# Kernel optimization log

Measured on AMD Instinct MI355X. Metric: run time of the kernel, lower is better.

The kernel has to match this reference:

```python
import jax, jax.numpy as jnp
import numpy as np
from jax import lax

DIM = 128
HEADS = 4
B, H, W = 8, 128, 128


def conv1x1(x, w, b):
    # x: [B,C,H,W], w: [O,I,1,1]
    y = lax.conv_general_dilated(x, w, (1, 1), 'VALID',
                                 dimension_numbers=('NCHW', 'OIHW', 'NCHW'))
    return y + b[None, :, None, None]


def dwconv3x3(x, w, b):
    # depthwise: w: [C,1,3,3], groups=C
    C = x.shape[1]
    y = lax.conv_general_dilated(x, w, (1, 1), ((1, 1), (1, 1)),
                                 dimension_numbers=('NCHW', 'OIHW', 'NCHW'),
                                 feature_group_count=C)
    return y + b[None, :, None, None]


def setup_inputs() -> dict:
    key = jax.random.key(0)
    ks = jax.random.split(key, 7)
    s = 0.02
    return {
        'x': jax.random.normal(ks[0], (B, DIM, H, W), jnp.float32),
        'qkv_w': jax.random.normal(ks[1], (3 * DIM, DIM, 1, 1), jnp.float32) * s,
        'qkv_b': jnp.zeros((3 * DIM,), jnp.float32),
        'dw_w': jax.random.normal(ks[2], (3 * DIM, 1, 3, 3), jnp.float32) * s,
        'dw_b': jnp.zeros((3 * DIM,), jnp.float32),
        'proj_w': jax.random.normal(ks[3], (DIM, DIM, 1, 1), jnp.float32) * s,
        'proj_b': jnp.zeros((DIM,), jnp.float32),
        'temperature': jnp.ones((HEADS, 1, 1, 1), jnp.float32),
    }


def reference(x, qkv_w, qkv_b, dw_w, dw_b, proj_w, proj_b, temperature):
    b, C, h, w = x.shape
    heads = temperature.shape[0]
    c = C // heads

    qkv = dwconv3x3(conv1x1(x, qkv_w, qkv_b), dw_w, dw_b)
    q, k, v = jnp.split(qkv, 3, axis=1)

    # b (head c) h w -> b head c h w
    q = q.reshape(b, heads, c, h, w)
    k = k.reshape(b, heads, c, h, w)
    v = v.reshape(b, heads, c, h, w)

    # L2-normalize along H (axis=-2), matching torch F.normalize eps=1e-12
    eps = 1e-12
    q = q / jnp.maximum(jnp.linalg.norm(q, axis=-2, keepdims=True), eps)
    k = k / jnp.maximum(jnp.linalg.norm(k, axis=-2, keepdims=True), eps)

    # attn[b,n,c,j,k] = sum_i q[b,n,c,i,j] * k_[b,n,c,i,k]  -> [b,head,c,W,W]
    attn = jnp.einsum('bncij,bncik->bncjk', q, k) * temperature
    attn = jax.nn.softmax(attn, axis=-2)

    # out[b,n,c,i,k] = sum_j v[b,n,c,i,j] * attn[b,n,c,j,k]
    out = jnp.einsum('bncij,bncjk->bncik', v, attn)
    out = out.reshape(b, C, h, w)
    return conv1x1(out, proj_w, proj_b)
```

## Files before the change

### kernel.cpp

```cpp
#include <hip/hip_runtime.h>

typedef unsigned short u16;
typedef unsigned int   u32;

typedef short bf16x8 __attribute__((ext_vector_type(8)));
typedef float f32x4  __attribute__((ext_vector_type(4)));

__device__ __forceinline__ float bf2f(u16 u) { return __uint_as_float(((u32)u) << 16); }
__device__ __forceinline__ u16 f2bf(float f) {
    u32 u = __float_as_uint(f);
    return (u16)((u + 0x7fffu + ((u >> 16) & 1u)) >> 16);
}

#define MFMA16(a, b, c) __builtin_amdgcn_mfma_f32_16x16x32_bf16(a, b, c, 0, 0, 0)

__global__ __launch_bounds__(256, 4) void k_xpose(const float* __restrict__ x,
                                                  u16* __restrict__ xT) {
    __shared__ u16 Xs[128 * 128];
    const int ptile = blockIdx.x, b = blockIdx.y;
    const int t = threadIdx.x;
    const float* xb = x + (((size_t)b) << 21) + ptile * 128;
#pragma unroll
    for (int i = 0; i < 16; ++i) {
        int idx = i * 256 + t;
        int ci = idx >> 5, pq = idx & 31;
        float4 v = *(const float4*)(xb + (((size_t)ci) << 14) + pq * 4);
        u32 lo = (u32)f2bf(v.x) | ((u32)f2bf(v.y) << 16);
        u32 hi = (u32)f2bf(v.z) | ((u32)f2bf(v.w) << 16);
        uint2 pk; pk.x = lo; pk.y = hi;
        int cq = ci >> 3;
        *(uint2*)(&Xs[ci * 128 + ((pq ^ cq) << 2)]) = pk;
    }
    __syncthreads();
    u16* ob = xT + (((size_t)b) << 21) + ((size_t)(ptile * 128)) * 128;
#pragma unroll
    for (int j = 0; j < 8; ++j) {
        int p = j * 16 + (t >> 4), cq = t & 15;
        u16 tmp[8];
#pragma unroll
        for (int c = 0; c < 8; ++c) {
            int ci = cq * 8 + c;
            tmp[c] = Xs[ci * 128 + (((p >> 2) ^ cq) << 2) + (p & 3)];
        }
        *(uint4*)(&ob[(size_t)p * 128 + cq * 8]) = *(const uint4*)tmp;
    }
}

__global__ __launch_bounds__(512, 6) void k_qkv(const u16* __restrict__ xT,
                                                const float* __restrict__ w,
                                                const float* __restrict__ bias,
                                                u16* __restrict__ out1) {
    extern __shared__ char smem[];
    u16* Bt = (u16*)smem;
    u16* Cs = Bt + 2048 * 8;
    const int h = blockIdx.x, cg = blockIdx.y, b = blockIdx.z;
    const int t = threadIdx.x;

    const u16* xb = xT + (((size_t)b) << 21) + ((size_t)(h * 128)) * 128;
#pragma unroll
    for (int i = 0; i < 4; ++i) {
        int slot = i * 512 + t;
        int p = slot >> 4, g = slot & 15;
        int gg = g ^ (p & 15);
        uint4 v = *(const uint4*)(&xb[p * 128 + gg * 8]);
        *(uint4*)(&Bt[slot * 8]) = v;
    }

    const int wave = t >> 6, lane = t & 63, m16 = lane & 15, quad = lane >> 4;
    bf16x8 afr[4];
    {
        const float* wp0 = w + (size_t)(cg * 128 + wave * 16 + m16) * 128 + quad * 8;
#pragma unroll
        for (int kk = 0; kk < 4; ++kk) {
            float4 w0 = *(const float4*)(wp0 + kk * 32);
            float4 w1 = *(const float4*)(wp0 + kk * 32 + 4);
            bf16x8 a;
            a[0] = (short)f2bf(w0.x); a[1] = (short)f2bf(w0.y);
            a[2] = (short)f2bf(w0.z); a[3] = (short)f2bf(w0.w);
            a[4] = (short)f2bf(w1.x); a[5] = (short)f2bf(w1.y);
            a[6] = (short)f2bf(w1.z); a[7] = (short)f2bf(w1.w);
            afr[kk] = a;
        }
    }
    __syncthreads();

    f32x4 acc[8] = {};
#pragma unroll
    for (int kk = 0; kk < 4; ++kk) {
        const int g = kk * 4 + quad;
#pragma unroll
        for (int nt = 0; nt < 8; ++nt) {
            int p = nt * 16 + m16;
            bf16x8 bf = *(const bf16x8*)(&Bt[p * 128 + ((g ^ (p & 15)) << 3)]);
            acc[nt] = MFMA16(afr[kk], bf, acc[nt]);
        }
    }

    float bv[4];
#pragma unroll
    for (int r = 0; r < 4; ++r) bv[r] = bias[cg * 128 + wave * 16 + quad * 4 + r];

    u16* ob = out1 + (((size_t)(b * 384 + cg * 128)) << 14) + (h << 7);

    if (wave < 4) {
#pragma unroll
        for (int nt = 0; nt < 8; ++nt) {
            int p = nt * 16 + m16;
#pragma unroll
            for (int r = 0; r < 4; ++r)
                Cs[(wave * 16 + quad * 4 + r) * 136 + p] = f2bf(acc[nt][r] + bv[r]);
        }
    }
    __syncthreads();
#pragma unroll
    for (int it = 0; it < 2; ++it) {
        int idx = it * 512 + t;
        int co = idx >> 4, cp = idx & 15;
        *(uint4*)(&ob[((size_t)co << 14) + cp * 8]) = *(const uint4*)(&Cs[co * 136 + cp * 8]);
    }
    __syncthreads();

    if (wave >= 4) {
#pragma unroll
        for (int nt = 0; nt < 8; ++nt) {
            int p = nt * 16 + m16;
#pragma unroll
            for (int r = 0; r < 4; ++r)
                Cs[((wave - 4) * 16 + quad * 4 + r) * 136 + p] = f2bf(acc[nt][r] + bv[r]);
        }
    }
    __syncthreads();
    u16* ob2 = ob + ((size_t)64 << 14);
#pragma unroll
    for (int it = 0; it < 2; ++it) {
        int idx = it * 512 + t;
        int co = idx >> 4, cp = idx & 15;
        *(uint4*)(&ob2[((size_t)co << 14) + cp * 8]) = *(const uint4*)(&Cs[co * 136 + cp * 8]);
    }
}

__global__ __launch_bounds__(512, 4) void k_attn(const u16* __restrict__ qkv,
                                                 const float* __restrict__ dww,
                                                 const float* __restrict__ dwb,
                                                 const float* __restrict__ temp,
                                                 u16* __restrict__ outp) {
    extern __shared__ char smem[];
    u16* Qt = (u16*)smem;
    u16* Kt = Qt + 16384;
    u16* Vr = (u16*)smem;
    u16* Sg2 = Qt + 32768;
    float* ps = (float*)(smem + 75904);
    float* rq = (float*)(smem + 77952);
    float* rk = (float*)(smem + 78464);
    u16* Pt = Qt;
    u16* Osh = Kt;

    const int ch = blockIdx.x, b = blockIdx.y;
    const int head = ch >> 5;
    const int t = threadIdx.x;
    const size_t qoff = ((size_t)(b * 384 + ch)) << 14;
    const size_t koff = qoff + ((size_t)128 << 14);
    const size_t voff = qoff + ((size_t)256 << 14);

    const int wave = t >> 6, lane = t & 63, m16 = lane & 15, quad = lane >> 4;

#pragma unroll
    for (int i = 0; i < 4; ++i) {
        int idx = i * 512 + t;
        int r = idx >> 4, c16 = idx & 15;
        *(uint4*)(&Vr[r * 144 + 8 + c16 * 8]) =
            *(const uint4*)(&qkv[voff + ((size_t)r << 7) + c16 * 8]);
    }
    if (t < 256) {
        int r = t >> 1, side = t & 1;
        uint4 z = {0, 0, 0, 0};
        *(uint4*)(&Vr[r * 144 + side * 136]) = z;
    } else if (t < 328) {
        int i = t - 256;
        int row = i >> 1, side = i & 1;
        uint4 z = {0, 0, 0, 0};
        *(uint4*)(&Sg2[row * 144 + side * 136]) = z;
    }
    __syncthreads();

    bf16x8 vfr[4];
    {
        float wv9[9];
        const float* wp = dww + (size_t)(256 + ch) * 9;
#pragma unroll
        for (int i = 0; i < 9; ++i) wv9[i] = wp[i];
        const float bvv = dwb[256 + ch];
        const int r = wave * 16 + m16;
#pragma unroll
        for (int kk = 0; kk < 4; ++kk) {
            const int c0 = quad * 8 + kk * 32;
            float acc[8];
#pragma unroll
            for (int c = 0; c < 8; ++c) acc[c] = bvv;
#pragma unroll
            for (int dy = 0; dy < 3; ++dy) {
                int rr = r + dy - 1;
                if ((unsigned)rr < 128u) {
                    const u16* row = &Vr[rr * 144 + 8 + c0];
                    float v0 = bf2f(row[-1]);
                    uint4 m = *(const uint4*)row;
                    float v1 = bf2f((u16)(m.x & 0xffff)), v2 = bf2f((u16)(m.x >> 16));
                    float v3 = bf2f((u16)(m.y & 0xffff)), v4 = bf2f((u16)(m.y >> 16));
                    float v5 = bf2f((u16)(m.z & 0xffff)), v6 = bf2f((u16)(m.z >> 16));
                    float v7 = bf2f((u16)(m.w & 0xffff)), v8 = bf2f((u16)(m.w >> 16));
                    float v9 = bf2f(row[8]);
                    const float w0 = wv9[dy * 3], w1 = wv9[dy * 3 + 1], w2 = wv9[dy * 3 + 2];
                    acc[0] += w0 * v0 + w1 * v1 + w2 * v2;
                    acc[1] += w0 * v1 + w1 * v2 + w2 * v3;
                    acc[2] += w0 * v2 + w1 * v3 + w2 * v4;
                    acc[3] += w0 * v3 + w1 * v4 + w2 * v5;
                    acc[4] += w0 * v4 + w1 * v5 + w2 * v6;
                    acc[5] += w0 * v5 + w1 * v6 + w2 * v7;
                    acc[6] += w0 * v6 + w1 * v7 + w2 * v8;
                    acc[7] += w0 * v7 + w1 * v8 + w2 * v9;
                }
            }
            bf16x8 a;
#pragma unroll
            for (int c = 0; c < 8; ++c) a[c] = (short)f2bf(acc[c]);
            vfr[kk] = a;
        }
    }
    __syncthreads();

    const int gmat = t >> 8, gig = (t >> 7) & 1, gj = t & 127;
    u16* gdstbase = (gmat ? Kt : Qt) + gj * 128;
    float wg9[9];
    {
        const float* wp = dww + (size_t)((gmat ? 128 : 0) + ch) * 9;
#pragma unroll
        for (int i = 0; i < 9; ++i) wg9[i] = wp[i];
    }
    const float gb = dwb[(gmat ? 128 : 0) + ch];
    float ssq = 0.f;

#pragma unroll 1
    for (int p = 0; p < 8; ++p) {
#pragma unroll
        for (int s0 = 0; s0 < 2; ++s0) {
            int s = s0 * 512 + t;
            if (s < 576) {
                int m = (s >= 288) ? 1 : 0;
                int within = s - m * 288;
                int lr = within >> 4, c16 = within & 15;
                int hh = p * 16 - 1 + lr;
                uint4 v = {0, 0, 0, 0};
                if ((unsigned)hh < 128u)
                    v = *(const uint4*)(&qkv[(m ? koff : qoff) + ((size_t)hh << 7) + c16 * 8]);
                *(uint4*)(&Sg2[(m * 18 + lr) * 144 + 8 + c16 * 8]) = v;
            }
        }
        __syncthreads();

        const u16* colp = &Sg2[(gmat * 18 + gig * 8) * 144 + 8 + gj];
        float acc[8];
#pragma unroll
        for (int c = 0; c < 8; ++c) acc[c] = gb;
#pragma unroll
        for (int lr = 0; lr < 10; ++lr) {
            const u16* rp = colp + lr * 144;
            float L = bf2f(rp[-1]);
            float C = bf2f(rp[0]);
            float R = bf2f(rp[1]);
            if (lr < 8) {
                float s0v = wg9[0] * L + wg9[1] * C + wg9[2] * R;
                acc[lr] += s0v;
            }
            if (lr >= 1 && lr <= 8) {
                float s1v = wg9[3] * L + wg9[4] * C + wg9[5] * R;
                acc[lr - 1] += s1v;
            }
            if (lr >= 2) {
                float s2v = wg9[6] * L + wg9[7] * C + wg9[8] * R;
                acc[lr - 2] += s2v;
            }
        }
        u16 tmp[8];
#pragma unroll
        for (int c = 0; c < 8; ++c) {
            u16 uv = f2bf(acc[c]);
            tmp[c] = uv;
            float f = bf2f(uv);
            ssq += f * f;
        }
        int g = p * 2 + gig;
        *(uint4*)(gdstbase + ((g ^ (gj & 15)) << 3)) = *(const uint4*)tmp;
        __syncthreads();
    }

    ps[(gmat * 2 + gig) * 128 + gj] = ssq;
    __syncthreads();
    if (t < 256) {
        int mat = t >> 7, j = t & 127;
        float s = ps[(mat * 2) * 128 + j] + ps[(mat * 2 + 1) * 128 + j];
        float r = 1.0f / fmaxf(sqrtf(s), 1e-12f);
        if (mat == 0) rq[j] = r; else rk[j] = r;
    }
    __syncthreads();

    f32x4 S[8] = {};
#pragma unroll
    for (int kk = 0; kk < 4; ++kk) {
        const int sw = ((kk * 4 + quad) ^ m16) << 3;
        bf16x8 bf = *(const bf16x8*)(&Kt[(wave * 16 + m16) * 128 + sw]);
#pragma unroll
        for (int jt = 0; jt < 8; ++jt) {
            bf16x8 af = *(const bf16x8*)(&Qt[(jt * 16 + m16) * 128 + sw]);
            S[jt] = MFMA16(af, bf, S[jt]);
        }
    }

    const float sc = temp[head] * rk[wave * 16 + m16];
    float vals[8][4];
    float vmax = -1e30f;
#pragma unroll
    for (int jt = 0; jt < 8; ++jt)
#pragma unroll
        for (int r = 0; r < 4; ++r) {
            float v = S[jt][r] * (rq[jt * 16 + quad * 4 + r] * sc);
            vals[jt][r] = v;
            vmax = fmaxf(vmax, v);
        }
    vmax = fmaxf(vmax, __shfl_xor(vmax, 16));
    vmax = fmaxf(vmax, __shfl_xor(vmax, 32));
    float sum = 0.f;
#pragma unroll
    for (int jt = 0; jt < 8; ++jt)
#pragma unroll
        for (int r = 0; r < 4; ++r) {
            float e = __expf(vals[jt][r] - vmax);
            vals[jt][r] = e;
            sum += e;
        }
    sum += __shfl_xor(sum, 16);
    sum += __shfl_xor(sum, 32);
    const float inv = 1.0f / sum;

    __syncthreads();

    {
        const int k = wave * 16 + m16;
        u16* prow = Pt + k * 128;
#pragma unroll
        for (int jt = 0; jt < 8; ++jt)
#pragma unroll
            for (int pr = 0; pr < 2; ++pr) {
                int j0 = jt * 16 + quad * 4 + pr * 2;
                u32 pk = (u32)f2bf(vals[jt][pr * 2] * inv) |
                         ((u32)f2bf(vals[jt][pr * 2 + 1] * inv) << 16);
                *(u32*)(prow + (((j0 >> 3) ^ (k & 15)) << 3) + (j0 & 7)) = pk;
            }
    }
    __syncthreads();

    f32x4 O[8] = {};
#pragma unroll
    for (int kk = 0; kk < 4; ++kk) {
        const int sw = ((kk * 4 + quad) ^ m16) << 3;
#pragma unroll
        for (int nt = 0; nt < 8; ++nt) {
            bf16x8 bf = *(const bf16x8*)(&Pt[(nt * 16 + m16) * 128 + sw]);
            O[nt] = MFMA16(vfr[kk], bf, O[nt]);
        }
    }

#pragma unroll
    for (int nt = 0; nt < 8; ++nt) {
        int k = nt * 16 + m16;
#pragma unroll
        for (int r = 0; r < 4; ++r) {
            int i = wave * 16 + quad * 4 + r;
            Osh[i * 128 + (((k >> 3) ^ (i & 15)) << 3) + (k & 7)] = f2bf(O[nt][r]);
        }
    }
    __syncthreads();

    u16* ob = outp + (((size_t)(b * 128 + ch)) << 14);
#pragma unroll
    for (int it = 0; it < 4; ++it) {
        int idx = it * 512 + t;
        int row = idx >> 4, gk = idx & 15;
        uint4 v = *(const uint4*)(&Osh[row * 128 + ((gk ^ (row & 15)) << 3)]);
        *(uint4*)(&ob[(row << 7) + gk * 8]) = v;
    }
}

__global__ __launch_bounds__(512, 6) void k_proj(const u16* __restrict__ ain,
                                                 const float* __restrict__ w,
                                                 const float* __restrict__ bias,
                                                 float* __restrict__ outp) {
    extern __shared__ char smem[];
    u16* Bt = (u16*)smem;
    u16* Sg = Bt + 16384;
    const int h = blockIdx.x, b = blockIdx.y;
    const int t = threadIdx.x;

    const int ldr = t >> 4, ldj8 = t & 15;
    const int gig = t >> 7, gp = t & 127;
    const u16* gcol = &Sg[(gig * 8) * 144 + gp];
    u16* gdst = Bt + gp * 128;
#pragma unroll
    for (int ph = 0; ph < 4; ++ph) {
        int ch = ph * 32 + ldr;
        *(uint4*)(&Sg[ldr * 144 + ldj8 * 8]) =
            *(const uint4*)(&ain[(((size_t)(b * 128 + ch)) << 14) + (h << 7) + ldj8 * 8]);
        __syncthreads();
        u16 tmp[8];
#pragma unroll
        for (int c = 0; c < 8; ++c) tmp[c] = gcol[c * 144];
        int g = ph * 4 + gig;
        *(uint4*)(gdst + ((g ^ (gp & 15)) << 3)) = *(const uint4*)tmp;
        __syncthreads();
    }

    const int wave = t >> 6, lane = t & 63, m16 = lane & 15, quad = lane >> 4;
    bf16x8 afr[4];
    {
        const float* wp0 = w + (size_t)(wave * 16 + m16) * 128 + quad * 8;
#pragma unroll
        for (int kk = 0; kk < 4; ++kk) {
            float4 w0 = *(const float4*)(wp0 + kk * 32);
            float4 w1 = *(const float4*)(wp0 + kk * 32 + 4);
            bf16x8 a;
            a[0] = (short)f2bf(w0.x); a[1] = (short)f2bf(w0.y);
            a[2] = (short)f2bf(w0.z); a[3] = (short)f2bf(w0.w);
            a[4] = (short)f2bf(w1.x); a[5] = (short)f2bf(w1.y);
            a[6] = (short)f2bf(w1.z); a[7] = (short)f2bf(w1.w);
            afr[kk] = a;
        }
    }

    f32x4 acc[8] = {};
#pragma unroll
    for (int kk = 0; kk < 4; ++kk) {
        const int g = kk * 4 + quad;
#pragma unroll
        for (int nt = 0; nt < 8; ++nt) {
            int p = nt * 16 + m16;
            bf16x8 bf = *(const bf16x8*)(&Bt[p * 128 + ((g ^ (p & 15)) << 3)]);
            acc[nt] = MFMA16(afr[kk], bf, acc[nt]);
        }
    }

    float bv[4];
#pragma unroll
    for (int r = 0; r < 4; ++r) bv[r] = bias[wave * 16 + quad * 4 + r];
    float* ob = outp + (((size_t)(b * 128)) << 14) + (h << 7);
#pragma unroll
    for (int nt = 0; nt < 8; ++nt) {
        int p = nt * 16 + m16;
#pragma unroll
        for (int r = 0; r < 4; ++r) {
            int co = wave * 16 + quad * 4 + r;
            ob[((size_t)co << 14) + p] = acc[nt][r] + bv[r];
        }
    }
}

extern "C" void kernel_launch(void* const* d_in, const int* in_sizes, int n_in,
                              void* d_out, int out_size, void* d_ws, size_t ws_size,
                              hipStream_t stream) {
    const float* x      = (const float*)d_in[0];
    const float* qkv_w  = (const float*)d_in[1];
    const float* qkv_b  = (const float*)d_in[2];
    const float* dw_w   = (const float*)d_in[3];
    const float* dw_b   = (const float*)d_in[4];
    const float* proj_w = (const float*)d_in[5];
    const float* proj_b = (const float*)d_in[6];
    const float* temp   = (const float*)d_in[7];
    float* out = (float*)d_out;

    u16* buf1 = (u16*)d_ws;
    u16* buf2 = buf1 + (size_t)8 * 384 * 16384;

    hipFuncSetAttribute((const void*)k_qkv,  hipFuncAttributeMaxDynamicSharedMemorySize, 50176);
    hipFuncSetAttribute((const void*)k_attn, hipFuncAttributeMaxDynamicSharedMemorySize, 78976);
    hipFuncSetAttribute((const void*)k_proj, hipFuncAttributeMaxDynamicSharedMemorySize, 41984);

    k_xpose<<<dim3(128, 8), 256, 0, stream>>>(x, buf2);
    k_qkv<<<dim3(128, 3, 8), 512, 50176, stream>>>(buf2, qkv_w, qkv_b, buf1);
    k_attn<<<dim3(128, 8), 512, 78976, stream>>>(buf1, dw_w, dw_b, temp, buf2);
    k_proj<<<dim3(128, 8), 512, 41984, stream>>>(buf2, proj_w, proj_b, out);
}
```

Baseline: 285.4 us.

## Store Q/K transposed from the qkv GEMM and vectorize the attention depthwise conv

The qkv 1x1-conv kernel is templated so the Q and K channel groups read the transposed input with a strided pattern and write Q/K with H and W swapped, while V keeps the old layout. The attention kernel then computes the Q/K depthwise 3x3 conv along contiguous rows using 16-byte shared-memory loads and 8-wide register sliding. It prefetches the next 34-row slab from global memory while computing the current one and reduces the L2 norms with warp shuffles instead of a shared partial-sum buffer. This is meant to cut the scalar shared-memory traffic and serialized load/compute phases of the old column-wise conv, and it slightly lowers shared memory use. The cost is strided global reads in the Q/K GEMM path and an extra kernel launch.

```diff
diff --git a/kernel.cpp b/kernel.cpp
--- a/kernel.cpp
+++ b/kernel.cpp
@@ -46,23 +46,25 @@
     }
 }
 
-__global__ __launch_bounds__(512, 6) void k_qkv(const u16* __restrict__ xT,
-                                                const float* __restrict__ w,
-                                                const float* __restrict__ bias,
-                                                u16* __restrict__ out1) {
+template <bool CM>
+__global__ __launch_bounds__(512, 6) void k_qkv_t(const u16* __restrict__ xT,
+                                                  const float* __restrict__ w,
+                                                  const float* __restrict__ bias,
+                                                  u16* __restrict__ out1,
+                                                  int cgbase) {
     extern __shared__ char smem[];
     u16* Bt = (u16*)smem;
     u16* Cs = Bt + 2048 * 8;
-    const int h = blockIdx.x, cg = blockIdx.y, b = blockIdx.z;
+    const int h = blockIdx.x, cg = blockIdx.y + cgbase, b = blockIdx.z;
     const int t = threadIdx.x;
 
-    const u16* xb = xT + (((size_t)b) << 21) + ((size_t)(h * 128)) * 128;
+    const u16* xb = xT + (((size_t)b) << 21) + (CM ? (h << 7) : (h << 14));
 #pragma unroll
     for (int i = 0; i < 4; ++i) {
         int slot = i * 512 + t;
         int p = slot >> 4, g = slot & 15;
         int gg = g ^ (p & 15);
-        uint4 v = *(const uint4*)(&xb[p * 128 + gg * 8]);
+        uint4 v = *(const uint4*)(&xb[(CM ? (p << 14) : (p << 7)) + gg * 8]);
         *(uint4*)(&Bt[slot * 8]) = v;
     }
 
@@ -148,10 +150,8 @@
     u16* Qt = (u16*)smem;
     u16* Kt = Qt + 16384;
     u16* Vr = (u16*)smem;
-    u16* Sg2 = Qt + 32768;
-    float* ps = (float*)(smem + 75904);
-    float* rq = (float*)(smem + 77952);
-    float* rk = (float*)(smem + 78464);
+    u16* Sg = Qt + 32768;
+    float* rqk = (float*)(smem + 75328);
     u16* Pt = Qt;
     u16* Osh = Kt;
 
@@ -175,11 +175,6 @@
         int r = t >> 1, side = t & 1;
         uint4 z = {0, 0, 0, 0};
         *(uint4*)(&Vr[r * 144 + side * 136]) = z;
-    } else if (t < 328) {
-        int i = t - 256;
-        int row = i >> 1, side = i & 1;
-        uint4 z = {0, 0, 0, 0};
-        *(uint4*)(&Sg2[row * 144 + side * 136]) = z;
     }
     __syncthreads();
 
@@ -228,59 +223,87 @@
     }
     __syncthreads();
 
-    const int gmat = t >> 8, gig = (t >> 7) & 1, gj = t & 127;
-    u16* gdstbase = (gmat ? Kt : Qt) + gj * 128;
-    float wg9[9];
+    if (t < 68) {
+        int r = t >> 1, side = t & 1;
+        uint4 z = {0, 0, 0, 0};
+        *(uint4*)(&Sg[r * 144 + side * 136]) = z;
+    }
+
+    const int sr = t >> 4, sc16 = t & 15;
+    const int jloc = t >> 4, seg = t & 15;
+
     {
-        const float* wp = dww + (size_t)((gmat ? 128 : 0) + ch) * 9;
-#pragma unroll
-        for (int i = 0; i < 9; ++i) wg9[i] = wp[i];
-    }
-    const float gb = dwb[(gmat ? 128 : 0) + ch];
-    float ssq = 0.f;
+        int grow = sr - 1;
+        uint4 v = {0, 0, 0, 0};
+        if ((unsigned)grow < 128u)
+            v = *(const uint4*)(&qkv[qoff + ((size_t)grow << 7) + sc16 * 8]);
+        *(uint4*)(&Sg[sr * 144 + 8 + sc16 * 8]) = v;
+        if (t < 32) {
+            int r2 = 32 + (t >> 4);
+            int g2 = r2 - 1;
+            uint4 v2 = {0, 0, 0, 0};
+            if ((unsigned)g2 < 128u)
+                v2 = *(const uint4*)(&qkv[qoff + ((size_t)g2 << 7) + sc16 * 8]);
+            *(uint4*)(&Sg[r2 * 144 + 8 + sc16 * 8]) = v2;
+        }
+    }
+    __syncthreads();
 
 #pragma unroll 1
-    for (int p = 0; p < 8; ++p) {
-#pragma unroll
-        for (int s0 = 0; s0 < 2; ++s0) {
-            int s = s0 * 512 + t;
-            if (s < 576) {
-                int m = (s >= 288) ? 1 : 0;
-                int within = s - m * 288;
-                int lr = within >> 4, c16 = within & 15;
-                int hh = p * 16 - 1 + lr;
-                uint4 v = {0, 0, 0, 0};
-                if ((unsigned)hh < 128u)
-                    v = *(const uint4*)(&qkv[(m ? koff : qoff) + ((size_t)hh << 7) + c16 * 8]);
-                *(uint4*)(&Sg2[(m * 18 + lr) * 144 + 8 + c16 * 8]) = v;
+    for (int ph = 0; ph < 8; ++ph) {
+        const int mat = ph >> 2;
+        const int j0 = (ph & 3) * 32;
+        const size_t moff = mat ? koff : qoff;
+
+        uint4 pf0 = {0, 0, 0, 0}, pf1 = {0, 0, 0, 0};
+        if (ph < 7) {
+            const int matn = (ph + 1) >> 2;
+            const int j0n = ((ph + 1) & 3) * 32;
+            const size_t moffn = matn ? koff : qoff;
+            int grow = j0n - 1 + sr;
+            if ((unsigned)grow < 128u)
+                pf0 = *(const uint4*)(&qkv[moffn + ((size_t)grow << 7) + sc16 * 8]);
+            if (t < 32) {
+                int g2 = j0n - 1 + 32 + (t >> 4);
+                if ((unsigned)g2 < 128u)
+                    pf1 = *(const uint4*)(&qkv[moffn + ((size_t)g2 << 7) + sc16 * 8]);
             }
         }
-        __syncthreads();
-
-        const u16* colp = &Sg2[(gmat * 18 + gig * 8) * 144 + 8 + gj];
+        (void)moff;
+
+        float wg9[9];
+        {
+            const float* wp = dww + (size_t)(mat * 128 + ch) * 9;
+#pragma unroll
+            for (int i = 0; i < 9; ++i) wg9[i] = wp[i];
+        }
+        const float gb = dwb[mat * 128 + ch];
+
         float acc[8];
 #pragma unroll
         for (int c = 0; c < 8; ++c) acc[c] = gb;
 #pragma unroll
-        for (int lr = 0; lr < 10; ++lr) {
-            const u16* rp = colp + lr * 144;
-            float L = bf2f(rp[-1]);
-            float C = bf2f(rp[0]);
-            float R = bf2f(rp[1]);
-            if (lr < 8) {
-                float s0v = wg9[0] * L + wg9[1] * C + wg9[2] * R;
-                acc[lr] += s0v;
-            }
-            if (lr >= 1 && lr <= 8) {
-                float s1v = wg9[3] * L + wg9[4] * C + wg9[5] * R;
-                acc[lr - 1] += s1v;
-            }
-            if (lr >= 2) {
-                float s2v = wg9[6] * L + wg9[7] * C + wg9[8] * R;
-                acc[lr - 2] += s2v;
-            }
+        for (int pr = 0; pr < 3; ++pr) {
+            const u16* row = &Sg[(jloc + pr) * 144 + 8 + seg * 8];
+            float v0 = bf2f(row[-1]);
+            uint4 m = *(const uint4*)row;
+            float v1 = bf2f((u16)(m.x & 0xffff)), v2 = bf2f((u16)(m.x >> 16));
+            float v3 = bf2f((u16)(m.y & 0xffff)), v4 = bf2f((u16)(m.y >> 16));
+            float v5 = bf2f((u16)(m.z & 0xffff)), v6 = bf2f((u16)(m.z >> 16));
+            float v7 = bf2f((u16)(m.w & 0xffff)), v8 = bf2f((u16)(m.w >> 16));
+            float v9 = bf2f(row[8]);
+            const float w0 = wg9[pr], w1 = wg9[3 + pr], w2 = wg9[6 + pr];
+            acc[0] += w0 * v0 + w1 * v1 + w2 * v2;
+            acc[1] += w0 * v1 + w1 * v2 + w2 * v3;
+            acc[2] += w0 * v2 + w1 * v3 + w2 * v4;
+            acc[3] += w0 * v3 + w1 * v4 + w2 * v5;
+            acc[4] += w0 * v4 + w1 * v5 + w2 * v6;
+            acc[5] += w0 * v5 + w1 * v6 + w2 * v7;
+            acc[6] += w0 * v6 + w1 * v7 + w2 * v8;
+            acc[7] += w0 * v7 + w1 * v8 + w2 * v9;
         }
         u16 tmp[8];
+        float ssq = 0.f;
 #pragma unroll
         for (int c = 0; c < 8; ++c) {
             u16 uv = f2bf(acc[c]);
@@ -288,19 +311,24 @@
             float f = bf2f(uv);
             ssq += f * f;
         }
-        int g = p * 2 + gig;
-        *(uint4*)(gdstbase + ((g ^ (gj & 15)) << 3)) = *(const uint4*)tmp;
+        ssq += __shfl_xor(ssq, 1);
+        ssq += __shfl_xor(ssq, 2);
+        ssq += __shfl_xor(ssq, 4);
+        ssq += __shfl_xor(ssq, 8);
+        const int j = j0 + jloc;
+        if (seg == 0) rqk[mat * 128 + j] = ssq;
+        u16* dst = (mat ? Kt : Qt) + j * 128 + ((seg ^ (j & 15)) << 3);
+        *(uint4*)dst = *(const uint4*)tmp;
+
         __syncthreads();
-    }
-
-    ps[(gmat * 2 + gig) * 128 + gj] = ssq;
-    __syncthreads();
-    if (t < 256) {
-        int mat = t >> 7, j = t & 127;
-        float s = ps[(mat * 2) * 128 + j] + ps[(mat * 2 + 1) * 128 + j];
-        float r = 1.0f / fmaxf(sqrtf(s), 1e-12f);
-        if (mat == 0) rq[j] = r; else rk[j] = r;
-    }
+        if (ph < 7) {
+            *(uint4*)(&Sg[sr * 144 + 8 + sc16 * 8]) = pf0;
+            if (t < 32) *(uint4*)(&Sg[(32 + (t >> 4)) * 144 + 8 + sc16 * 8]) = pf1;
+        }
+        __syncthreads();
+    }
+
+    if (t < 256) rqk[t] = 1.0f / fmaxf(sqrtf(rqk[t]), 1e-12f);
     __syncthreads();
 
     f32x4 S[8] = {};
@@ -315,14 +343,14 @@
         }
     }
 
-    const float sc = temp[head] * rk[wave * 16 + m16];
+    const float sc = temp[head] * rqk[128 + wave * 16 + m16];
     float vals[8][4];
     float vmax = -1e30f;
 #pragma unroll
     for (int jt = 0; jt < 8; ++jt)
 #pragma unroll
         for (int r = 0; r < 4; ++r) {
-            float v = S[jt][r] * (rq[jt * 16 + quad * 4 + r] * sc);
+            float v = S[jt][r] * (rqk[jt * 16 + quad * 4 + r] * sc);
             vals[jt][r] = v;
             vmax = fmaxf(vmax, v);
         }
@@ -350,10 +378,10 @@
         for (int jt = 0; jt < 8; ++jt)
 #pragma unroll
             for (int pr = 0; pr < 2; ++pr) {
-                int j0 = jt * 16 + quad * 4 + pr * 2;
+                int j0w = jt * 16 + quad * 4 + pr * 2;
                 u32 pk = (u32)f2bf(vals[jt][pr * 2] * inv) |
                          ((u32)f2bf(vals[jt][pr * 2 + 1] * inv) << 16);
-                *(u32*)(prow + (((j0 >> 3) ^ (k & 15)) << 3) + (j0 & 7)) = pk;
+                *(u32*)(prow + (((j0w >> 3) ^ (k & 15)) << 3) + (j0w & 7)) = pk;
             }
     }
     __syncthreads();
@@ -478,12 +506,14 @@
     u16* buf1 = (u16*)d_ws;
     u16* buf2 = buf1 + (size_t)8 * 384 * 16384;
 
-    hipFuncSetAttribute((const void*)k_qkv,  hipFuncAttributeMaxDynamicSharedMemorySize, 50176);
-    hipFuncSetAttribute((const void*)k_attn, hipFuncAttributeMaxDynamicSharedMemorySize, 78976);
+    hipFuncSetAttribute((const void*)k_qkv_t<true>,  hipFuncAttributeMaxDynamicSharedMemorySize, 50176);
+    hipFuncSetAttribute((const void*)k_qkv_t<false>, hipFuncAttributeMaxDynamicSharedMemorySize, 50176);
+    hipFuncSetAttribute((const void*)k_attn, hipFuncAttributeMaxDynamicSharedMemorySize, 76352);
     hipFuncSetAttribute((const void*)k_proj, hipFuncAttributeMaxDynamicSharedMemorySize, 41984);
 
     k_xpose<<<dim3(128, 8), 256, 0, stream>>>(x, buf2);
-    k_qkv<<<dim3(128, 3, 8), 512, 50176, stream>>>(buf2, qkv_w, qkv_b, buf1);
-    k_attn<<<dim3(128, 8), 512, 78976, stream>>>(buf1, dw_w, dw_b, temp, buf2);
+    k_qkv_t<true><<<dim3(128, 2, 8), 512, 50176, stream>>>(buf2, qkv_w, qkv_b, buf1, 0);
+    k_qkv_t<false><<<dim3(128, 1, 8), 512, 50176, stream>>>(buf2, qkv_w, qkv_b, buf1, 2);
+    k_attn<<<dim3(128, 8), 512, 76352, stream>>>(buf1, dw_w, dw_b, temp, buf2);
     k_proj<<<dim3(128, 8), 512, 41984, stream>>>(buf2, proj_w, proj_b, out);
 }
```

Measured after the change: 248.0 us. -13.1%, faster.
